# Kernel tuning notes

Measured on AMD Instinct MI355X. Metric: run time of the kernel, lower is better.

The kernel has to match this reference:

```python
import jax, jax.numpy as jnp
import numpy as np

N_ITEMS = 50000
N_USERS = 20000
N_NODES = N_ITEMS + N_USERS
D = 128
N_REL = 3
NNZ = 800000
K_LAYERS = 2
B, S, L = 256, 4, 50


def setup_inputs() -> dict:
    key = jax.random.key(0)
    ks = iter(jax.random.split(key, 40))
    stdv = float(1.0 / np.sqrt(D))

    def uni(shape):
        return jax.random.uniform(next(ks), shape, jnp.float32, -stdv, stdv)

    id_emb = (jax.random.normal(next(ks), (N_ITEMS, D), jnp.float32) * 0.1).at[0].set(0.0)  # padding_idx=0
    user_emb = jax.random.normal(next(ks), (N_USERS, D), jnp.float32) * 0.1
    inp = dict(
        id_emb=id_emb, user_emb=user_emb,
        lin_r_w=uni((K_LAYERS, N_REL, D, D)),
        upi_w=uni((K_LAYERS, D, D)), upi_b=uni((K_LAYERS, D)),
        upu_w=uni((K_LAYERS, D, D)), upu_b=uni((K_LAYERS, D)),
        w_ih=uni((3 * D, 2 * D)), w_hh=uni((3 * D, D)),
        b_ih=uni((3 * D,)), b_hh=uni((3 * D,)),
        b_iah=uni((D,)), b_oah=uni((D,)),
        ei_w=uni((D, D)), ei_b=uni((D,)),
        eo_w=uni((D, D)), eo_b=uni((D,)),
        q1_w=uni((D, D)), q2_w=uni((D, D)), att_w=uni((D,)),
        fuse_w=uni((D, 2 * D)), fuse_b=uni((D,)),
    )
    # global heterogeneous graph: COO per relation over item+user nodes
    inp['rel_rows'] = jax.random.randint(next(ks), (N_REL, NNZ), 0, N_NODES, dtype=jnp.int32)
    inp['rel_cols'] = jax.random.randint(next(ks), (N_REL, NNZ), 0, N_NODES, dtype=jnp.int32)
    inp['rel_vals'] = jax.random.uniform(next(ks), (N_REL, NNZ), jnp.float32) * 0.1
    # session batch: every session has length in [2, L]
    lens = jax.random.randint(next(ks), (B, S), 2, L + 1)
    raw = jax.random.randint(next(ks), (B, S, L), 1, N_ITEMS)
    inp['ids'] = (raw * (jnp.arange(L)[None, None, :] < lens[:, :, None])).astype(jnp.int32)
    inp['uid'] = jax.random.randint(next(ks), (B,), 0, N_USERS, dtype=jnp.int32)
    inp['u_type'] = jax.random.randint(next(ks), (B,), 0, 3).astype(jnp.float32)
    return inp


def _hgnn(h_item, h_user, rel_rows, rel_cols, rel_vals, lin_r_w, upi_w, upi_b, upu_w, upu_b):
    Ni = h_item.shape[0]
    N = Ni + h_user.shape[0]
    for k in range(lin_r_w.shape[0]):
        h_all = jnp.concatenate([h_item, h_user], 0)
        msg = jnp.zeros_like(h_all)
        for r in range(rel_rows.shape[0]):
            Wh = h_all @ lin_r_w[k, r].T  # per-relation linear
            msg = msg + jax.ops.segment_sum(Wh[rel_cols[r]] * rel_vals[r][:, None],
                                            rel_rows[r], num_segments=N)  # sparse.mm
        h_item = jax.nn.relu((msg[:Ni] + h_item) @ upi_w[k].T + upi_b[k])
        h_user = jax.nn.relu((msg[Ni:] + h_user) @ upu_w[k].T + upu_b[k])
    return h_item, h_user


def reference(id_emb, user_emb, lin_r_w, upi_w, upi_b, upu_w, upu_b,
              w_ih, w_hh, b_ih, b_hh, b_iah, b_oah,
              ei_w, ei_b, eo_w, eo_b, q1_w, q2_w, att_w, fuse_w, fuse_b,
              rel_rows, rel_cols, rel_vals, ids, uid, u_type):
    Bb, Ss, Ll = ids.shape
    N = Ss * Bb
    ids_sb = jnp.transpose(ids, (1, 0, 2)).reshape(N, Ll)  # session-major, matches torch concat order
    lens = (ids_sb != 0).sum(-1)  # >= 2 by construction -> all sessions valid
    rows = jnp.arange(N)
    target = ids_sb[rows, lens - 1]
    Lp = Ll - 1
    m_in = jnp.arange(Lp)[None, :] < (lens - 1)[:, None]
    seq_in = ids_sb[:, :Lp] * m_in
    # session graph: consecutive-item edges; in-half sub-diagonal, out-half super-diagonal
    valid = (m_in[:, 1:] & m_in[:, :-1]).astype(jnp.float32)  # [N, Lp-1]
    i1 = jnp.arange(1, Lp)
    i0 = jnp.arange(Lp - 1)
    a_in = jnp.zeros((N, Lp, Lp), jnp.float32).at[:, i1, i0].set(valid)
    a_out = jnp.zeros((N, Lp, Lp), jnp.float32).at[:, i0, i1].set(valid)
    deg = jnp.clip(a_in.sum(-1), 1.0, None)[..., None]
    a_in = a_in / deg
    a_out = a_out / deg
    h = id_emb[seq_in]  # [N, Lp, D]
    # SessionGNN GRU-style cell (step=1)
    m_i = jnp.matmul(a_in, h @ ei_w.T + ei_b) + b_iah
    m_o = jnp.matmul(a_out, h @ eo_w.T + eo_b) + b_oah
    gi = jnp.concatenate([m_i, m_o], -1) @ w_ih.T + b_ih
    gh = h @ w_hh.T + b_hh
    i_r, i_i, i_n = jnp.split(gi, 3, -1)
    h_r, h_i, h_n = jnp.split(gh, 3, -1)
    rg = jax.nn.sigmoid(i_r + h_r)
    zg = jax.nn.sigmoid(i_i + h_i)
    ng = jnp.tanh(i_n + rg * h_n)
    h = ng + zg * (h - ng)
    # attention readout
    ht = h[rows, jnp.clip(lens - 2, 0, None)]
    alpha = jax.nn.sigmoid((ht @ q1_w.T)[:, None, :] + h @ q2_w.T) @ att_w  # [N, Lp]
    alpha = alpha * m_in.astype(jnp.float32)
    alpha = alpha / (alpha.sum(1, keepdims=True) + 1e-8)
    c_cur = jnp.einsum('nl,nld->nd', alpha, h)
    # global HGNN user context
    g_item, g_user = _hgnn(id_emb[:N_ITEMS], user_emb[:N_USERS], rel_rows, rel_cols,
                           rel_vals, lin_r_w, upi_w, upi_b, upu_w, upu_b)
    c_hist = g_user[jnp.tile(uid, Ss)]
    reps = jnp.concatenate([c_cur, c_hist], -1) @ fuse_w.T + fuse_b
    return reps, target, jnp.tile(u_type, Ss)
```

## Files before the change

### kernel.cpp

```cpp
#include <hip/hip_runtime.h>
#include <hip/hip_bf16.h>

typedef __hip_bfloat16 bf16;
typedef unsigned int uint32;
typedef __attribute__((ext_vector_type(8))) short short8;
typedef __attribute__((ext_vector_type(4))) float f32x4;
typedef __attribute__((ext_vector_type(2))) float f32x2;
typedef __attribute__((ext_vector_type(4))) uint32 u32x4;

#define N_ITEMS_C 50000
#define N_USERS_C 20000
#define N_NODES_C 70000
#define NNZ_C 800000
#define NSESS 1024
#define LP 49
#define NTOK (NSESS * LP)
#define NBK 137

__device__ __forceinline__ float bflo(uint32 u) { return __uint_as_float(u << 16); }
__device__ __forceinline__ float bfhi(uint32 u) { return __uint_as_float(u & 0xffff0000u); }
__device__ __forceinline__ float bfhi_fast(uint32 u) { return __uint_as_float(u); }
__device__ __forceinline__ uint32 packbf(float a, float b) {
    return (uint32)__bfloat16_as_ushort(__float2bfloat16(a)) |
           ((uint32)__bfloat16_as_ushort(__float2bfloat16(b)) << 16);
}

__global__ void init_hab_kernel(const float4* __restrict__ idp, const float4* __restrict__ usp,
                                uint32* __restrict__ hab) {
    int i = blockIdx.x * 256 + threadIdx.x;
    float4 w = (i < 1600000) ? idp[i] : usp[i - 1600000];
    uint2 o = make_uint2(packbf(w.x, w.y), packbf(w.z, w.w));
    *(uint2*)&hab[(size_t)i * 2] = o;
}

__global__ __launch_bounds__(256) void bucket_hist_kernel(
    const int* __restrict__ rel_rows, int* __restrict__ bhist)
{
    __shared__ int hist[NBK];
    const int r = blockIdx.y, tid = threadIdx.x;
    if (tid < NBK) hist[tid] = 0;
    __syncthreads();
    const int* rr = rel_rows + (size_t)r * NNZ_C;
#pragma unroll
    for (int i = 0; i < 16; ++i) {
        int e = blockIdx.x * 4096 + i * 256 + tid;
        if (e < NNZ_C) atomicAdd(&hist[rr[e] >> 9], 1);
    }
    __syncthreads();
    if (tid < NBK && hist[tid]) atomicAdd(&bhist[r * NBK + tid], hist[tid]);
}

__global__ __launch_bounds__(256) void bucket_scan_kernel(
    const int* __restrict__ bhist, int* __restrict__ bbase)
{
    __shared__ int s[256];
    const int tid = threadIdx.x;
    for (int r = 0; r < 3; ++r) {
        s[tid] = (tid < NBK) ? bhist[r * NBK + tid] : 0;
        __syncthreads();
        for (int d = 1; d < 256; d <<= 1) {
            int t = (tid >= d) ? s[tid - d] : 0;
            __syncthreads();
            s[tid] += t;
            __syncthreads();
        }
        if (tid < NBK) bbase[r * (NBK + 1) + tid + 1] = s[tid];
        if (tid == 0) bbase[r * (NBK + 1)] = 0;
        __syncthreads();
    }
}

__global__ __launch_bounds__(256) void bucket_scatter_kernel(
    const int* __restrict__ rel_rows, const int* __restrict__ rel_cols,
    const float* __restrict__ rel_vals, const int* __restrict__ bbase,
    int* __restrict__ cursor, int2* __restrict__ tmp)
{
    __shared__ int hist[NBK], gbase[NBK], cur2[NBK];
    const int r = blockIdx.y, tid = threadIdx.x;
    if (tid < NBK) { hist[tid] = 0; cur2[tid] = 0; }
    __syncthreads();
    const int* rr = rel_rows + (size_t)r * NNZ_C;
    const int* rc = rel_cols + (size_t)r * NNZ_C;
    const float* rv = rel_vals + (size_t)r * NNZ_C;
    int rows[16];
#pragma unroll
    for (int i = 0; i < 16; ++i) {
        int e = blockIdx.x * 4096 + i * 256 + tid;
        rows[i] = (e < NNZ_C) ? rr[e] : -1;
        if (rows[i] >= 0) atomicAdd(&hist[rows[i] >> 9], 1);
    }
    __syncthreads();
    if (tid < NBK)
        gbase[tid] = bbase[r * (NBK + 1) + tid] +
                     (hist[tid] ? atomicAdd(&cursor[r * NBK + tid], hist[tid]) : 0);
    __syncthreads();
    int2* tp = tmp + (size_t)r * NNZ_C;
#pragma unroll
    for (int i = 0; i < 16; ++i) {
        int e = blockIdx.x * 4096 + i * 256 + tid;
        if (rows[i] >= 0) {
            int bk = rows[i] >> 9;
            int rank = atomicAdd(&cur2[bk], 1);
            uint32 fb = __float_as_uint(rv[e]);
            uint32 pk = (uint32)rc[e] | (((fb >> 16) & 0x7FFFu) << 17);
            tp[gbase[bk] + rank] = make_int2((int)pk, rows[i]);
        }
    }
}

__global__ __launch_bounds__(256) void bucket_refine_kernel(
    const int2* __restrict__ tmp, const int* __restrict__ bbase,
    int* __restrict__ offs, uint32* __restrict__ edges)
{
    __shared__ int cnt[512], offsL[512], cur[512];
    __shared__ uint32 outb[6656];
    const int b = blockIdx.x, r = blockIdx.y, tid = threadIdx.x;
    const int lane = tid & 63, wid = tid >> 6;
    const int row0 = b << 9;
    const int e0 = bbase[r * (NBK + 1) + b];
    const int e1 = bbase[r * (NBK + 1) + b + 1];
    cnt[tid] = 0; cnt[256 + tid] = 0; cur[tid] = 0; cur[256 + tid] = 0;
    __syncthreads();
    const int2* tp = tmp + (size_t)r * NNZ_C;
    for (int e = e0 + tid; e < e1; e += 256)
        atomicAdd(&cnt[tp[e].y - row0], 1);
    __syncthreads();
    if (wid == 0) {
        int carry = 0;
        for (int c = 0; c < 8; ++c) {
            int x = cnt[c * 64 + lane];
            int inc = x;
#pragma unroll
            for (int d = 1; d < 64; d <<= 1) {
                int y = __shfl_up(inc, d, 64);
                if (lane >= d) inc += y;
            }
            offsL[c * 64 + lane] = inc - x + carry;
            carry += __shfl(inc, 63, 64);
        }
    }
    __syncthreads();
    for (int i = tid; i < 512; i += 256) {
        int row = row0 + i;
        if (row < 70001) offs[(size_t)r * 70001 + row] = e0 + offsL[i];
    }
    for (int e = e0 + tid; e < e1; e += 256) {
        int2 E = tp[e];
        int lr_ = E.y - row0;
        int slot = offsL[lr_] + atomicAdd(&cur[lr_], 1);
        if (slot < 6656) outb[slot] = (uint32)E.x;
    }
    __syncthreads();
    uint32* eo = edges + (size_t)r * NNZ_C + e0;
    for (int i = tid; i < e1 - e0; i += 256) eo[i] = outb[i];
}

__global__ __launch_bounds__(256) void gather_kernel(
    const uint32* __restrict__ hab, const uint32* __restrict__ edges,
    const int* __restrict__ offs, uint32* __restrict__ T)
{
    const int row = blockIdx.x * 4 + (threadIdx.x >> 6);
    const int lane = threadIdx.x & 63;
    const int grp = lane >> 4;
    const int ql  = lane & 15;
    const char* __restrict__ habB = (const char*)hab + ql * 16;
    f32x2 acc[3][4];
#pragma unroll
    for (int r = 0; r < 3; ++r)
#pragma unroll
        for (int j = 0; j < 4; ++j) acc[r][j] = (f32x2){0.f, 0.f};
#pragma unroll
    for (int r = 0; r < 3; ++r) {
        const uint32* __restrict__ ed = edges + (size_t)r * NNZ_C;
        const int* __restrict__ of = offs + (size_t)r * 70001;
        const int e0 = of[row], e1 = of[row + 1];
        if (e0 >= e1) continue;
        const uint32 span = (uint32)(e1 - e0);
        const int s0 = e0 & ~3;
        for (int eb = s0; eb < e1; eb += 16) {
            const int base = eb + grp * 4;
            uint4 E4 = *(const uint4*)&ed[base];
            uint32 Ej0 = ((uint32)(base + 0 - e0) < span) ? E4.x : 0u;
            uint32 Ej1 = ((uint32)(base + 1 - e0) < span) ? E4.y : 0u;
            uint32 Ej2 = ((uint32)(base + 2 - e0) < span) ? E4.z : 0u;
            uint32 Ej3 = ((uint32)(base + 3 - e0) < span) ? E4.w : 0u;
            uint4 u0 = *(const uint4*)(habB + ((Ej0 & 0x1FFFFu) << 8));
            uint4 u1 = *(const uint4*)(habB + ((Ej1 & 0x1FFFFu) << 8));
            uint4 u2 = *(const uint4*)(habB + ((Ej2 & 0x1FFFFu) << 8));
            uint4 u3 = *(const uint4*)(habB + ((Ej3 & 0x1FFFFu) << 8));
            float v0 = __uint_as_float((Ej0 >> 1) & 0x7FFF0000u);
            float v1 = __uint_as_float((Ej1 >> 1) & 0x7FFF0000u);
            float v2 = __uint_as_float((Ej2 >> 1) & 0x7FFF0000u);
            float v3 = __uint_as_float((Ej3 >> 1) & 0x7FFF0000u);
            f32x2 vv;
            vv = (f32x2){v0, v0};
            acc[r][0] += vv * (f32x2){bflo(u0.x), bfhi_fast(u0.x)};
            acc[r][1] += vv * (f32x2){bflo(u0.y), bfhi_fast(u0.y)};
            acc[r][2] += vv * (f32x2){bflo(u0.z), bfhi_fast(u0.z)};
            acc[r][3] += vv * (f32x2){bflo(u0.w), bfhi_fast(u0.w)};
            vv = (f32x2){v1, v1};
            acc[r][0] += vv * (f32x2){bflo(u1.x), bfhi_fast(u1.x)};
            acc[r][1] += vv * (f32x2){bflo(u1.y), bfhi_fast(u1.y)};
            acc[r][2] += vv * (f32x2){bflo(u1.z), bfhi_fast(u1.z)};
            acc[r][3] += vv * (f32x2){bflo(u1.w), bfhi_fast(u1.w)};
            vv = (f32x2){v2, v2};
            acc[r][0] += vv * (f32x2){bflo(u2.x), bfhi_fast(u2.x)};
            acc[r][1] += vv * (f32x2){bflo(u2.y), bfhi_fast(u2.y)};
            acc[r][2] += vv * (f32x2){bflo(u2.z), bfhi_fast(u2.z)};
            acc[r][3] += vv * (f32x2){bflo(u2.w), bfhi_fast(u2.w)};
            vv = (f32x2){v3, v3};
            acc[r][0] += vv * (f32x2){bflo(u3.x), bfhi_fast(u3.x)};
            acc[r][1] += vv * (f32x2){bflo(u3.y), bfhi_fast(u3.y)};
            acc[r][2] += vv * (f32x2){bflo(u3.z), bfhi_fast(u3.z)};
            acc[r][3] += vv * (f32x2){bflo(u3.w), bfhi_fast(u3.w)};
        }
    }
    float* af = (float*)acc;
#pragma unroll
    for (int off = 16; off < 64; off <<= 1)
#pragma unroll
        for (int j = 0; j < 24; ++j) af[j] += __shfl_xor(af[j], off, 64);
    if (grp == 0) {
#pragma unroll
        for (int r = 0; r < 3; ++r) {
            u32x4 o;
            o.x = packbf(acc[r][0].x, acc[r][0].y);
            o.y = packbf(acc[r][1].x, acc[r][1].y);
            o.z = packbf(acc[r][2].x, acc[r][2].y);
            o.w = packbf(acc[r][3].x, acc[r][3].y);
            __builtin_nontemporal_store(o, (u32x4*)&T[(size_t)row * 192 + r * 64 + ql * 4]);
        }
    }
}

__global__ __launch_bounds__(256, 3) void wprep_kernel(
    const float* __restrict__ upi_w, const float* __restrict__ upu_w,
    const float* __restrict__ lin_r_w, int k, uint32* __restrict__ Wcat)
{
    __shared__ float As[128][65];
    __shared__ __align__(8) bf16 Ws[128][66];
    const int which = blockIdx.y, seg = which / 3, r = which % 3;
    const float* U  = (seg == 0 ? upi_w : upu_w) + (size_t)k * 16384;
    const float* Wr = lin_r_w + (size_t)(k * 3 + r) * 16384;
    uint32* out = Wcat + (size_t)seg * 32768;
    const int tid = threadIdx.x;
    const int row0 = blockIdx.x * 64;
#pragma unroll
    for (int i = 0; i < 8; ++i) {
        int id = i * 256 + tid;
        int rr = id >> 5, c4 = (id & 31) << 2;
        float4 v = *(const float4*)&U[(size_t)(row0 + rr) * 128 + c4];
        As[c4][rr] = v.x; As[c4+1][rr] = v.y; As[c4+2][rr] = v.z; As[c4+3][rr] = v.w;
    }
    const int m0 = (tid & 15) * 4;
    const int n0 = (tid >> 4) * 8;
    float acc[4][8];
#pragma unroll
    for (int i = 0; i < 4; ++i)
#pragma unroll
        for (int j = 0; j < 8; ++j) acc[i][j] = 0.f;
    for (int p = 0; p < 2; ++p) {
        if (p) __syncthreads();
        for (int i = 0; i < 32; ++i) {
            int id = i * 256 + tid;
            int c = id >> 6, kf = id & 63;
            Ws[c][kf] = __float2bfloat16(Wr[(size_t)(p * 64 + kf) * 128 + c]);
        }
        __syncthreads();
        for (int k2 = 0; k2 < 32; ++k2) {
            int kk = p * 64 + 2 * k2;
            float av0[4], av1[4];
#pragma unroll
            for (int i = 0; i < 4; ++i) { av0[i] = As[kk][m0 + i]; av1[i] = As[kk + 1][m0 + i]; }
#pragma unroll
            for (int j = 0; j < 8; ++j) {
                uint32 wp = *(const uint32*)&Ws[n0 + j][2 * k2];
                float w0 = bflo(wp), w1 = bfhi(wp);
#pragma unroll
                for (int i = 0; i < 4; ++i)
                    acc[i][j] = fmaf(av1[i], w1, fmaf(av0[i], w0, acc[i][j]));
            }
        }
    }
#pragma unroll
    for (int i = 0; i < 4; ++i) {
        int n = row0 + m0 + i;
#pragma unroll
        for (int j = 0; j < 8; j += 2)
            out[(size_t)n * 256 + (r * 128 + n0 + j) / 2] = packbf(acc[i][j], acc[i][j + 1]);
    }
}

__global__ __launch_bounds__(256) void upack_kernel(
    const float* __restrict__ upi_w, const float* __restrict__ upu_w,
    int k, uint32* __restrict__ Wcat)
{
    int id = blockIdx.x * 256 + threadIdx.x;
    int seg = id >> 13, p = id & 8191;
    int n = p >> 6, j2 = (p & 63);
    const float* U = (seg ? upu_w : upi_w) + (size_t)k * 16384;
    float2 w = *(const float2*)&U[(size_t)n * 128 + j2 * 2];
    Wcat[(size_t)seg * 32768 + (size_t)n * 256 + 192 + j2] = packbf(w.x, w.y);
}

#define HGNN_ITEM_BLOCKS 391
__global__ __launch_bounds__(256) void hgnn_update_mfma_kernel(
    const bf16* __restrict__ T, uint32* __restrict__ hab,
    const bf16* __restrict__ Wcat, const float* __restrict__ upi_b,
    const float* __restrict__ upu_b, int k)
{
    const int tid = threadIdx.x;
    const int wv = tid >> 6, lane = tid & 63, quad = lane >> 4, lr = lane & 15;
    const int bid = blockIdx.x;
    const int seg = (bid >= HGNN_ITEM_BLOCKS) ? 1 : 0;
    const int row0 = seg ? N_ITEMS_C : 0;
    const int M = seg ? N_USERS_C : N_ITEMS_C;
    const int rbase = (seg ? bid - HGNN_ITEM_BLOCKS : bid) * 128;
    const bf16* __restrict__ Wc = Wcat + (size_t)seg * 65536;
    const float* __restrict__ bias = (seg ? upu_b : upi_b) + k * 128;
    const bf16* hb = (const bf16*)hab;
    f32x4 acc[8][2];
#pragma unroll
    for (int mt = 0; mt < 8; ++mt) { acc[mt][0] = (f32x4){0,0,0,0}; acc[mt][1] = (f32x4){0,0,0,0}; }
    int arow[8];
#pragma unroll
    for (int mt = 0; mt < 8; ++mt) {
        int rr = rbase + mt * 16 + lr;
        arow[mt] = row0 + (rr < M ? rr : M - 1);
    }
#pragma unroll
    for (int ks = 0; ks < 16; ++ks) {
        short8 b0 = *(const short8*)&Wc[(size_t)(wv * 32 + lr) * 512 + ks * 32 + quad * 8];
        short8 b1 = *(const short8*)&Wc[(size_t)(wv * 32 + 16 + lr) * 512 + ks * 32 + quad * 8];
#pragma unroll
        for (int mt = 0; mt < 8; ++mt) {
            short8 a;
            if (ks < 12) a = *(const short8*)&T[(size_t)arow[mt] * 384 + ks * 32 + quad * 8];
            else         a = *(const short8*)&hb[(size_t)arow[mt] * 128 + (ks - 12) * 32 + quad * 8];
            acc[mt][0] = __builtin_amdgcn_mfma_f32_16x16x32_bf16(a, b0, acc[mt][0], 0, 0, 0);
            acc[mt][1] = __builtin_amdgcn_mfma_f32_16x16x32_bf16(a, b1, acc[mt][1], 0, 0, 0);
        }
    }
    __syncthreads();
    unsigned short* hw = (unsigned short*)hab;
#pragma unroll
    for (int s = 0; s < 2; ++s) {
        int col = wv * 32 + s * 16 + lr;
        float bv = bias[col];
#pragma unroll
        for (int mt = 0; mt < 8; ++mt)
#pragma unroll
            for (int reg = 0; reg < 4; ++reg) {
                int rr = rbase + mt * 16 + quad * 4 + reg;
                if (rr < M) {
                    float v = fmaxf(acc[mt][s][reg] + bv, 0.f);
                    hw[(size_t)(row0 + rr) * 128 + col] = __bfloat16_as_ushort(__float2bfloat16(v));
                }
            }
    }
}

__global__ __launch_bounds__(256) void mfma_nt_kernel(
    const bf16* __restrict__ A, const int* __restrict__ rowmap,
    const bf16* __restrict__ W0, const float* __restrict__ b0,
    float* __restrict__ O0, int M)
{
    const int tid = threadIdx.x;
    const int wv = tid >> 6, lane = tid & 63, quad = lane >> 4, lr = lane & 15;
    const int rbase = blockIdx.x * 128;
    int arow[8];
#pragma unroll
    for (int mt = 0; mt < 8; ++mt) {
        int rr = rbase + mt * 16 + lr;
        rr = rr < M ? rr : M - 1;
        arow[mt] = rowmap ? rowmap[rr] : rr;
    }
    f32x4 acc0[8][2];
#pragma unroll
    for (int mt = 0; mt < 8; ++mt) { acc0[mt][0] = (f32x4){0,0,0,0}; acc0[mt][1] = (f32x4){0,0,0,0}; }
#pragma unroll
    for (int ks = 0; ks < 4; ++ks) {
        short8 b00 = *(const short8*)&W0[(size_t)(wv * 32 + lr) * 128 + ks * 32 + quad * 8];
        short8 b01 = *(const short8*)&W0[(size_t)(wv * 32 + 16 + lr) * 128 + ks * 32 + quad * 8];
#pragma unroll
        for (int mt = 0; mt < 8; ++mt) {
            short8 a = *(const short8*)&A[(size_t)arow[mt] * 128 + ks * 32 + quad * 8];
            acc0[mt][0] = __builtin_amdgcn_mfma_f32_16x16x32_bf16(a, b00, acc0[mt][0], 0, 0, 0);
            acc0[mt][1] = __builtin_amdgcn_mfma_f32_16x16x32_bf16(a, b01, acc0[mt][1], 0, 0, 0);
        }
    }
#pragma unroll
    for (int s = 0; s < 2; ++s) {
        int col = wv * 32 + s * 16 + lr;
        float bv0 = b0 ? b0[col] : 0.f;
#pragma unroll
        for (int mt = 0; mt < 8; ++mt)
#pragma unroll
            for (int reg = 0; reg < 4; ++reg) {
                int rr = rbase + mt * 16 + quad * 4 + reg;
                if (rr < M) O0[(size_t)rr * 128 + col] = acc0[mt][s][reg] + bv0;
            }
    }
}

__global__ void session_prep_kernel(const int* __restrict__ ids, const int* __restrict__ uid,
                                    const float* __restrict__ u_type,
                                    int* __restrict__ lens, int* __restrict__ rowmap,
                                    float* __restrict__ out_target, float* __restrict__ out_utype)
{
    int n = blockIdx.x * 256 + threadIdx.x;
    if (n >= NSESS) return;
    int b = n & 255, s = n >> 8;
    const int* row = ids + (size_t)(b * 4 + s) * 50;
    int len = 0;
#pragma unroll
    for (int l = 0; l < 50; ++l) len += (row[l] != 0) ? 1 : 0;
    lens[n] = len;
    rowmap[n] = n * LP + (len - 2);
    out_target[n] = (float)row[len - 1];
    out_utype[n] = u_type[b];
}

__global__ void chist_kernel(const uint32* __restrict__ hab, const int* __restrict__ uid,
                             float* __restrict__ chist) {
    int n = blockIdx.x, d = threadIdx.x;
    uint32 u = hab[(size_t)(N_ITEMS_C + uid[n & 255]) * 64 + (d >> 1)];
    chist[(size_t)n * 128 + d] = (d & 1) ? bfhi(u) : bflo(u);
}

__global__ __launch_bounds__(256) void h0_gather_kernel(
    const float* __restrict__ id_emb, const int* __restrict__ ids,
    const int* __restrict__ lens, uint32* __restrict__ hb) {
    int g = blockIdx.x * 4 + (threadIdx.x >> 6);
    int d = threadIdx.x & 63;
    int n = g / LP;
    int tt = g - n * LP;
    int len = lens[n];
    int b = n & 255, s = n >> 8;
    int id = (tt < len - 1) ? ids[(size_t)(b * 4 + s) * 50 + tt] : 0;
    float2 e = *(const float2*)&id_emb[(size_t)id * 128 + d * 2];
    hb[(size_t)g * 64 + d] = packbf(e.x, e.y);
}

__global__ __launch_bounds__(256) void epack_kernel(
    const float* __restrict__ w_ih, const float* __restrict__ w_hh,
    const float* __restrict__ ei_w, const float* __restrict__ eo_w,
    const float* __restrict__ q2_w, const float* __restrict__ q1_w,
    const float* __restrict__ fuse_w, uint32* __restrict__ dst)
{
    int id = blockIdx.x * 256 + threadIdx.x;
    if (id >= 106496) {
        if (id >= 139264) return;
        int f = id - 106496;
        int kk = f >> 7, n = f & 127;
        ((float*)dst)[id] = fuse_w[(size_t)n * 256 + kk];
        return;
    }
    const float* src; int off;
    if      (id <  49152) { src = w_ih; off = id; }
    else if (id <  73728) { src = w_hh; off = id - 49152; }
    else if (id <  81920) { src = ei_w; off = id - 73728; }
    else if (id <  90112) { src = eo_w; off = id - 81920; }
    else if (id <  98304) { src = q2_w; off = id - 90112; }
    else                  { src = q1_w; off = id - 98304; }
    float2 w = *(const float2*)&src[(size_t)off * 2];
    dst[id] = packbf(w.x, w.y);
}

__global__ __launch_bounds__(256) void gru_fused_kernel(
    const uint32* __restrict__ hb,
    unsigned short* __restrict__ hb2,
    const bf16* __restrict__ Wi, const bf16* __restrict__ Wo,
    const bf16* __restrict__ wihb,
    const bf16* __restrict__ whhb,
    const float* __restrict__ ei_b, const float* __restrict__ eo_b,
    const float* __restrict__ b_iah, const float* __restrict__ b_oah,
    const float* __restrict__ b_ih, const float* __restrict__ b_hh,
    const int* __restrict__ lens)
{
    __shared__ __align__(16) bf16 Agi[32][264];
    const int tid = threadIdx.x;
    const int wv = tid >> 6;
    const int lane = tid & 63;
    const int quad = lane >> 4;
    const int lr = lane & 15;
    const int c0 = wv * 32;
    const int g0 = blockIdx.x * 32;
    const bf16* hbb = (const bf16*)hb;

    int arows[4];
#pragma unroll
    for (int t = 0; t < 4; ++t) {
        int r = g0 + (t - 1) * 16 + lr;
        arows[t] = (r < 0) ? r + NTOK : (r >= NTOK ? r - NTOK : r);
    }
    f32x4 aEi[3][2], aEo[3][2];
#pragma unroll
    for (int t = 0; t < 3; ++t) {
        aEi[t][0] = (f32x4){0,0,0,0}; aEi[t][1] = (f32x4){0,0,0,0};
        aEo[t][0] = (f32x4){0,0,0,0}; aEo[t][1] = (f32x4){0,0,0,0};
    }
#pragma unroll
    for (int ks = 0; ks < 4; ++ks) {
        short8 bi0 = *(const short8*)&Wi[(size_t)(wv * 32 + lr) * 128 + ks * 32 + quad * 8];
        short8 bi1 = *(const short8*)&Wi[(size_t)(wv * 32 + 16 + lr) * 128 + ks * 32 + quad * 8];
        short8 bo0 = *(const short8*)&Wo[(size_t)(wv * 32 + lr) * 128 + ks * 32 + quad * 8];
        short8 bo1 = *(const short8*)&Wo[(size_t)(wv * 32 + 16 + lr) * 128 + ks * 32 + quad * 8];
        short8 a[4];
#pragma unroll
        for (int t = 0; t < 4; ++t)
            a[t] = *(const short8*)&hbb[(size_t)arows[t] * 128 + ks * 32 + quad * 8];
#pragma unroll
        for (int t = 0; t < 3; ++t) {
            aEi[t][0] = __builtin_amdgcn_mfma_f32_16x16x32_bf16(a[t], bi0, aEi[t][0], 0, 0, 0);
            aEi[t][1] = __builtin_amdgcn_mfma_f32_16x16x32_bf16(a[t], bi1, aEi[t][1], 0, 0, 0);
            aEo[t][0] = __builtin_amdgcn_mfma_f32_16x16x32_bf16(a[t + 1], bo0, aEo[t][0], 0, 0, 0);
            aEo[t][1] = __builtin_amdgcn_mfma_f32_16x16x32_bf16(a[t + 1], bo1, aEo[t][1], 0, 0, 0);
        }
    }
#pragma unroll
    for (int s = 0; s < 2; ++s) {
        int col = c0 + s * 16 + lr;
        float bei = ei_b[col], beo = eo_b[col];
        float bia = b_iah[col], boa = b_oah[col];
#pragma unroll
        for (int t = 0; t < 3; ++t)
#pragma unroll
            for (int reg = 0; reg < 4; ++reg) {
                int src = g0 + (t - 1) * 16 + quad * 4 + reg;
                int ssrc = (src < 0) ? src + NTOK : (src >= NTOK ? src - NTOK : src);
                int d1 = ssrc + 1; if (d1 == NTOK) d1 = 0;
                int ld = d1 - g0;
                if ((unsigned)ld < 32u) {
                    int n1 = d1 / LP, t1 = d1 - n1 * LP, l1 = lens[n1];
                    float v = bia + ((t1 >= 1 && t1 < l1 - 1) ? aEi[t][s][reg] + bei : 0.f);
                    Agi[ld][col] = __float2bfloat16(v);
                }
                int src2 = g0 + t * 16 + quad * 4 + reg;
                int ssrc2 = (src2 >= NTOK) ? src2 - NTOK : src2;
                int d2 = (ssrc2 == 0) ? NTOK - 1 : ssrc2 - 1;
                int ld2 = d2 - g0;
                if ((unsigned)ld2 < 32u) {
                    int n2 = d2 / LP, t2 = d2 - n2 * LP, l2 = lens[n2];
                    float v = boa + ((t2 < l2 - 2) ? aEo[t][s][reg] + beo : 0.f);
                    Agi[ld2][128 + col] = __float2bfloat16(v);
                }
            }
    }
    __syncthreads();

    int arow[2];
#pragma unroll
    for (int mt = 0; mt < 2; ++mt) arow[mt] = g0 + mt * 16 + lr;
    f32x4 acc[2][2][4];
#pragma unroll
    for (int mt = 0; mt < 2; ++mt)
#pragma unroll
        for (int s = 0; s < 2; ++s)
#pragma unroll
            for (int j = 0; j < 4; ++j) acc[mt][s][j] = (f32x4){0.f, 0.f, 0.f, 0.f};

#pragma unroll 2
    for (int ks = 0; ks < 8; ++ks) {
        short8 bfr[2][3];
#pragma unroll
        for (int s = 0; s < 2; ++s)
#pragma unroll
            for (int gte = 0; gte < 3; ++gte) {
                int n0 = gte * 128 + c0 + s * 16 + lr;
                bfr[s][gte] = *(const short8*)&wihb[(size_t)n0 * 256 + ks * 32 + quad * 8];
            }
#pragma unroll
        for (int mt = 0; mt < 2; ++mt) {
            short8 a = *(const short8*)&Agi[mt * 16 + lr][ks * 32 + quad * 8];
#pragma unroll
            for (int s = 0; s < 2; ++s) {
                acc[mt][s][0] = __builtin_amdgcn_mfma_f32_16x16x32_bf16(a, bfr[s][0], acc[mt][s][0], 0, 0, 0);
                acc[mt][s][1] = __builtin_amdgcn_mfma_f32_16x16x32_bf16(a, bfr[s][1], acc[mt][s][1], 0, 0, 0);
                acc[mt][s][2] = __builtin_amdgcn_mfma_f32_16x16x32_bf16(a, bfr[s][2], acc[mt][s][2], 0, 0, 0);
            }
        }
    }
#pragma unroll 2
    for (int ks = 0; ks < 4; ++ks) {
        short8 bfr[2][3];
#pragma unroll
        for (int s = 0; s < 2; ++s)
#pragma unroll
            for (int gte = 0; gte < 3; ++gte) {
                int n0 = gte * 128 + c0 + s * 16 + lr;
                bfr[s][gte] = *(const short8*)&whhb[(size_t)n0 * 128 + ks * 32 + quad * 8];
            }
#pragma unroll
        for (int mt = 0; mt < 2; ++mt) {
            short8 a = *(const short8*)&hbb[(size_t)arow[mt] * 128 + ks * 32 + quad * 8];
#pragma unroll
            for (int s = 0; s < 2; ++s) {
                acc[mt][s][0] = __builtin_amdgcn_mfma_f32_16x16x32_bf16(a, bfr[s][0], acc[mt][s][0], 0, 0, 0);
                acc[mt][s][1] = __builtin_amdgcn_mfma_f32_16x16x32_bf16(a, bfr[s][1], acc[mt][s][1], 0, 0, 0);
                acc[mt][s][3] = __builtin_amdgcn_mfma_f32_16x16x32_bf16(a, bfr[s][2], acc[mt][s][3], 0, 0, 0);
            }
        }
    }

    const unsigned short* hold = (const unsigned short*)hb;
#pragma unroll
    for (int s = 0; s < 2; ++s) {
        int col = c0 + s * 16 + lr;
        float brz = b_ih[col] + b_hh[col];
        float bzz = b_ih[col + 128] + b_hh[col + 128];
        float bin = b_ih[col + 256];
        float bhn = b_hh[col + 256];
#pragma unroll
        for (int mt = 0; mt < 2; ++mt)
#pragma unroll
            for (int reg = 0; reg < 4; ++reg) {
                int row = g0 + mt * 16 + quad * 4 + reg;
                float rg = 1.f / (1.f + expf(-(acc[mt][s][0][reg] + brz)));
                float zg = 1.f / (1.f + expf(-(acc[mt][s][1][reg] + bzz)));
                float ng = tanhf(acc[mt][s][2][reg] + bin + rg * (acc[mt][s][3][reg] + bhn));
                size_t idx = (size_t)row * 128 + col;
                float ho = __uint_as_float((uint32)hold[idx] << 16);
                hb2[idx] = __bfloat16_as_ushort(__float2bfloat16(ng + zg * (ho - ng)));
            }
    }
}

__global__ __launch_bounds__(256) void alpha_kernel(
    const float* __restrict__ q1h, const float* __restrict__ q2h,
    const float* __restrict__ att_w, const int* __restrict__ lens,
    float* __restrict__ al)
{
    int tok = blockIdx.x * 4 + (threadIdx.x >> 6);
    int lane = threadIdx.x & 63;
    int n = tok / LP, t = tok - n * LP;
    int len = lens[n];
    float2 q2 = *(const float2*)&q2h[(size_t)tok * 128 + lane * 2];
    float2 q1 = *(const float2*)&q1h[(size_t)n * 128 + lane * 2];
    float2 aw = *(const float2*)&att_w[lane * 2];
    float s = aw.x / (1.f + expf(-(q1.x + q2.x))) + aw.y / (1.f + expf(-(q1.y + q2.y)));
#pragma unroll
    for (int off = 1; off < 64; off <<= 1) s += __shfl_xor(s, off, 64);
    if (lane == 0) al[tok] = (t < len - 1) ? s : 0.f;
}

__global__ __launch_bounds__(128) void attn_fuse_kernel(
    const float* __restrict__ alG, const unsigned short* __restrict__ hu,
    const float* __restrict__ chist, const int* __restrict__ lens,
    const float* __restrict__ ftwf, const float* __restrict__ fuse_b,
    float* __restrict__ out)
{
    __shared__ float al[64], cv[256];
    const int n = blockIdx.x, tid = threadIdx.x;
    if (tid < 64) al[tid] = (tid < LP) ? alG[(size_t)n * LP + tid] : 0.f;
    __syncthreads();
    const int len = lens[n];
    float ssum = 0.f;
    for (int t = 0; t < len - 1; ++t) ssum += al[t];
    float inv = 1.f / (ssum + 1e-8f);
    float c = 0.f;
    for (int t = 0; t < len - 1; ++t) {
        float hv = __uint_as_float((uint32)hu[(size_t)(n * LP + t) * 128 + tid] << 16);
        c += al[t] * inv * hv;
    }
    cv[tid] = c;
    cv[128 + tid] = chist[(size_t)n * 128 + tid];
    __syncthreads();
    float s = fuse_b[tid];
    for (int kk = 0; kk < 256; ++kk)
        s += cv[kk] * ftwf[(size_t)kk * 128 + tid];
    out[(size_t)n * 128 + tid] = s;
}

extern "C" void kernel_launch(void* const* d_in, const int* in_sizes, int n_in,
                              void* d_out, int out_size, void* d_ws, size_t ws_size,
                              hipStream_t stream)
{
    const float* id_emb   = (const float*)d_in[0];
    const float* user_emb = (const float*)d_in[1];
    const float* lin_r_w  = (const float*)d_in[2];
    const float* upi_w    = (const float*)d_in[3];
    const float* upi_b    = (const float*)d_in[4];
    const float* upu_w    = (const float*)d_in[5];
    const float* upu_b    = (const float*)d_in[6];
    const float* w_ih     = (const float*)d_in[7];
    const float* w_hh     = (const float*)d_in[8];
    const float* b_ih     = (const float*)d_in[9];
    const float* b_hh     = (const float*)d_in[10];
    const float* b_iah    = (const float*)d_in[11];
    const float* b_oah    = (const float*)d_in[12];
    const float* ei_w     = (const float*)d_in[13];
    const float* ei_b     = (const float*)d_in[14];
    const float* eo_w     = (const float*)d_in[15];
    const float* eo_b     = (const float*)d_in[16];
    const float* q1_w     = (const float*)d_in[17];
    const float* q2_w     = (const float*)d_in[18];
    const float* att_w    = (const float*)d_in[19];
    const float* fuse_w   = (const float*)d_in[20];
    const float* fuse_b   = (const float*)d_in[21];
    const int*  rel_rows  = (const int*)d_in[22];
    const int*  rel_cols  = (const int*)d_in[23];
    const float* rel_vals = (const float*)d_in[24];
    const int*  ids       = (const int*)d_in[25];
    const int*  uid       = (const int*)d_in[26];
    const float* u_type   = (const float*)d_in[27];
    float* out = (float*)d_out;

    uint32* W32    = (uint32*)d_ws;
    uint32* hab    = W32;
    uint32* T      = W32 + 4480000;
    uint32* edges  = W32 + 17920000;
    int2*   tmp    = (int2*)(W32 + 20320000);
    int*    offs   = (int*)(W32 + 25120000);
    int*    bhist  = (int*)(W32 + 25330004);
    int*    cursor = (int*)(W32 + 25330415);
    int*    bbase  = (int*)(W32 + 25330826);
    uint32* Wcat   = W32 + 25331240;
    float*  q1h    = (float*)(W32 + 25396776);
    float*  chist  = (float*)(W32 + 25527848);
    int*    lens   = (int*)(W32 + 25658920);
    int*    rowmap = (int*)(W32 + 25659944);
    float*  alG    = (float*)(W32 + 25660968);
    uint32* sess_hb = W32;
    float* q2h      = (float*)(W32 + 4480000);
    unsigned short* hb2 = (unsigned short*)(W32 + 10902528);
    uint32* wpk     = W32 + 17920000;
    uint32* wihb = wpk;
    uint32* whhb = wpk + 49152;
    uint32* eiwb = wpk + 73728;
    uint32* eowb = wpk + 81920;
    uint32* q2wb = wpk + 90112;
    uint32* q1wb = wpk + 98304;
    float*  ftwf = (float*)(wpk + 106496);
    if (ws_size < (size_t)27144192 * 4 + 4096) return;

    init_hab_kernel<<<8750, 256, 0, stream>>>((const float4*)id_emb, (const float4*)user_emb, hab);
    hipMemsetAsync(bhist, 0, (size_t)822 * 4, stream);
    bucket_hist_kernel<<<dim3(196, 3), 256, 0, stream>>>(rel_rows, bhist);
    bucket_scan_kernel<<<1, 256, 0, stream>>>(bhist, bbase);
    bucket_scatter_kernel<<<dim3(196, 3), 256, 0, stream>>>(rel_rows, rel_cols, rel_vals,
                                                            bbase, cursor, tmp);
    bucket_refine_kernel<<<dim3(NBK, 3), 256, 0, stream>>>(tmp, bbase, offs, edges);

    for (int k = 0; k < 2; ++k) {
        wprep_kernel<<<dim3(2, 6), 256, 0, stream>>>(upi_w, upu_w, lin_r_w, k, Wcat);
        upack_kernel<<<64, 256, 0, stream>>>(upi_w, upu_w, k, Wcat);
        gather_kernel<<<17500, 256, 0, stream>>>(hab, edges, offs, T);
        hgnn_update_mfma_kernel<<<548, 256, 0, stream>>>((const bf16*)T, hab,
            (const bf16*)Wcat, upi_b, upu_b, k);
    }

    session_prep_kernel<<<4, 256, 0, stream>>>(ids, uid, u_type, lens, rowmap,
        out + 131072, out + 132096);
    chist_kernel<<<NSESS, 128, 0, stream>>>(hab, uid, chist);
    epack_kernel<<<544, 256, 0, stream>>>(w_ih, w_hh, ei_w, eo_w, q2_w, q1_w, fuse_w, wpk);
    h0_gather_kernel<<<NTOK / 4, 256, 0, stream>>>(id_emb, ids, lens, sess_hb);
    gru_fused_kernel<<<1568, 256, 0, stream>>>(sess_hb, hb2,
        (const bf16*)eiwb, (const bf16*)eowb,
        (const bf16*)wihb, (const bf16*)whhb,
        ei_b, eo_b, b_iah, b_oah, b_ih, b_hh, lens);
    mfma_nt_kernel<<<392, 256, 0, stream>>>((const bf16*)hb2, nullptr,
        (const bf16*)q2wb, nullptr, q2h, NTOK);
    mfma_nt_kernel<<<8, 256, 0, stream>>>((const bf16*)hb2, rowmap,
        (const bf16*)q1wb, nullptr, q1h, NSESS);
    alpha_kernel<<<NTOK / 4, 256, 0, stream>>>(q1h, q2h, att_w, lens, alG);
    attn_fuse_kernel<<<NSESS, 128, 0, stream>>>(alG, (const unsigned short*)hb2,
        chist, lens, ftwf, fuse_b, out);
}
```

Baseline: 748.2 us.

## Fuse q2 projection with alpha scoring and merge small prep kernels

Fuses the q2 GEMM with the sigmoid/attention-weight reduction so the NTOK×128 fp32 q2h intermediate is never written or read back. Merges init_hab with bucket histogram, and session prep, chist, weight packing and h0 gather into single launches. Weight prep for both HGNN layers is hoisted out of the loop into one launch each, and h0 gather computes length with a ballot. The aim is fewer launches and less memory traffic, at the cost of buffer relocation in the workspace and more divergent monolithic kernels.

```diff
diff --git a/kernel.cpp b/kernel.cpp
--- a/kernel.cpp
+++ b/kernel.cpp
@@ -25,25 +25,27 @@
            ((uint32)__bfloat16_as_ushort(__float2bfloat16(b)) << 16);
 }
 
-__global__ void init_hab_kernel(const float4* __restrict__ idp, const float4* __restrict__ usp,
-                                uint32* __restrict__ hab) {
-    int i = blockIdx.x * 256 + threadIdx.x;
-    float4 w = (i < 1600000) ? idp[i] : usp[i - 1600000];
-    uint2 o = make_uint2(packbf(w.x, w.y), packbf(w.z, w.w));
-    *(uint2*)&hab[(size_t)i * 2] = o;
-}
-
-__global__ __launch_bounds__(256) void bucket_hist_kernel(
-    const int* __restrict__ rel_rows, int* __restrict__ bhist)
+__global__ __launch_bounds__(256) void init_hist_kernel(
+    const float4* __restrict__ idp, const float4* __restrict__ usp,
+    uint32* __restrict__ hab, const int* __restrict__ rel_rows, int* __restrict__ bhist)
 {
     __shared__ int hist[NBK];
-    const int r = blockIdx.y, tid = threadIdx.x;
+    const int tid = threadIdx.x;
+    if (blockIdx.x < 8750) {
+        int i = blockIdx.x * 256 + tid;
+        float4 w = (i < 1600000) ? idp[i] : usp[i - 1600000];
+        uint2 o = make_uint2(packbf(w.x, w.y), packbf(w.z, w.w));
+        *(uint2*)&hab[(size_t)i * 2] = o;
+        return;
+    }
+    const int hb = blockIdx.x - 8750;
+    const int r = hb / 196, xb = hb - r * 196;
     if (tid < NBK) hist[tid] = 0;
     __syncthreads();
     const int* rr = rel_rows + (size_t)r * NNZ_C;
 #pragma unroll
     for (int i = 0; i < 16; ++i) {
-        int e = blockIdx.x * 4096 + i * 256 + tid;
+        int e = xb * 4096 + i * 256 + tid;
         if (e < NNZ_C) atomicAdd(&hist[rr[e] >> 9], 1);
     }
     __syncthreads();
@@ -235,14 +237,15 @@
 
 __global__ __launch_bounds__(256, 3) void wprep_kernel(
     const float* __restrict__ upi_w, const float* __restrict__ upu_w,
-    const float* __restrict__ lin_r_w, int k, uint32* __restrict__ Wcat)
+    const float* __restrict__ lin_r_w, uint32* __restrict__ Wcat)
 {
     __shared__ float As[128][65];
     __shared__ __align__(8) bf16 Ws[128][66];
     const int which = blockIdx.y, seg = which / 3, r = which % 3;
+    const int k = blockIdx.z;
     const float* U  = (seg == 0 ? upi_w : upu_w) + (size_t)k * 16384;
     const float* Wr = lin_r_w + (size_t)(k * 3 + r) * 16384;
-    uint32* out = Wcat + (size_t)seg * 32768;
+    uint32* out = Wcat + (size_t)(k * 2 + seg) * 32768;
     const int tid = threadIdx.x;
     const int row0 = blockIdx.x * 64;
 #pragma unroll
@@ -293,14 +296,15 @@
 
 __global__ __launch_bounds__(256) void upack_kernel(
     const float* __restrict__ upi_w, const float* __restrict__ upu_w,
-    int k, uint32* __restrict__ Wcat)
+    uint32* __restrict__ Wcat)
 {
     int id = blockIdx.x * 256 + threadIdx.x;
-    int seg = id >> 13, p = id & 8191;
+    int k = id >> 14, rest = id & 16383;
+    int seg = rest >> 13, p = rest & 8191;
     int n = p >> 6, j2 = (p & 63);
     const float* U = (seg ? upu_w : upi_w) + (size_t)k * 16384;
     float2 w = *(const float2*)&U[(size_t)n * 128 + j2 * 2];
-    Wcat[(size_t)seg * 32768 + (size_t)n * 256 + 192 + j2] = packbf(w.x, w.y);
+    Wcat[(size_t)(k * 2 + seg) * 32768 + (size_t)n * 256 + 192 + j2] = packbf(w.x, w.y);
 }
 
 #define HGNN_ITEM_BLOCKS 391
@@ -316,7 +320,7 @@
     const int row0 = seg ? N_ITEMS_C : 0;
     const int M = seg ? N_USERS_C : N_ITEMS_C;
     const int rbase = (seg ? bid - HGNN_ITEM_BLOCKS : bid) * 128;
-    const bf16* __restrict__ Wc = Wcat + (size_t)seg * 65536;
+    const bf16* __restrict__ Wc = Wcat + (size_t)(k * 2 + seg) * 65536;
     const float* __restrict__ bias = (seg ? upu_b : upi_b) + k * 128;
     const bf16* hb = (const bf16*)hab;
     f32x4 acc[8][2];
@@ -403,68 +407,73 @@
     }
 }
 
-__global__ void session_prep_kernel(const int* __restrict__ ids, const int* __restrict__ uid,
-                                    const float* __restrict__ u_type,
-                                    int* __restrict__ lens, int* __restrict__ rowmap,
-                                    float* __restrict__ out_target, float* __restrict__ out_utype)
-{
-    int n = blockIdx.x * 256 + threadIdx.x;
-    if (n >= NSESS) return;
-    int b = n & 255, s = n >> 8;
-    const int* row = ids + (size_t)(b * 4 + s) * 50;
-    int len = 0;
-#pragma unroll
-    for (int l = 0; l < 50; ++l) len += (row[l] != 0) ? 1 : 0;
-    lens[n] = len;
-    rowmap[n] = n * LP + (len - 2);
-    out_target[n] = (float)row[len - 1];
-    out_utype[n] = u_type[b];
-}
-
-__global__ void chist_kernel(const uint32* __restrict__ hab, const int* __restrict__ uid,
-                             float* __restrict__ chist) {
-    int n = blockIdx.x, d = threadIdx.x;
-    uint32 u = hab[(size_t)(N_ITEMS_C + uid[n & 255]) * 64 + (d >> 1)];
-    chist[(size_t)n * 128 + d] = (d & 1) ? bfhi(u) : bflo(u);
-}
-
-__global__ __launch_bounds__(256) void h0_gather_kernel(
-    const float* __restrict__ id_emb, const int* __restrict__ ids,
-    const int* __restrict__ lens, uint32* __restrict__ hb) {
-    int g = blockIdx.x * 4 + (threadIdx.x >> 6);
-    int d = threadIdx.x & 63;
-    int n = g / LP;
-    int tt = g - n * LP;
-    int len = lens[n];
-    int b = n & 255, s = n >> 8;
-    int id = (tt < len - 1) ? ids[(size_t)(b * 4 + s) * 50 + tt] : 0;
-    float2 e = *(const float2*)&id_emb[(size_t)id * 128 + d * 2];
-    hb[(size_t)g * 64 + d] = packbf(e.x, e.y);
-}
-
-__global__ __launch_bounds__(256) void epack_kernel(
+__global__ __launch_bounds__(256) void misc_prep_kernel(
+    const int* __restrict__ ids, const int* __restrict__ uid,
+    const float* __restrict__ u_type, const float* __restrict__ id_emb,
+    const uint32* __restrict__ hab,
     const float* __restrict__ w_ih, const float* __restrict__ w_hh,
     const float* __restrict__ ei_w, const float* __restrict__ eo_w,
     const float* __restrict__ q2_w, const float* __restrict__ q1_w,
-    const float* __restrict__ fuse_w, uint32* __restrict__ dst)
-{
-    int id = blockIdx.x * 256 + threadIdx.x;
-    if (id >= 106496) {
-        if (id >= 139264) return;
-        int f = id - 106496;
-        int kk = f >> 7, n = f & 127;
-        ((float*)dst)[id] = fuse_w[(size_t)n * 256 + kk];
+    const float* __restrict__ fuse_w,
+    int* __restrict__ lens, int* __restrict__ rowmap,
+    float* __restrict__ out_target, float* __restrict__ out_utype,
+    float* __restrict__ chist, uint32* __restrict__ wdst,
+    uint32* __restrict__ hb)
+{
+    const int bid = blockIdx.x, tid = threadIdx.x;
+    if (bid < 4) {
+        int n = bid * 256 + tid;
+        if (n >= NSESS) return;
+        int b = n & 255, s = n >> 8;
+        const int* row = ids + (size_t)(b * 4 + s) * 50;
+        int len = 0;
+#pragma unroll
+        for (int l = 0; l < 50; ++l) len += (row[l] != 0) ? 1 : 0;
+        lens[n] = len;
+        rowmap[n] = n * LP + (len - 2);
+        out_target[n] = (float)row[len - 1];
+        out_utype[n] = u_type[b];
         return;
     }
-    const float* src; int off;
-    if      (id <  49152) { src = w_ih; off = id; }
-    else if (id <  73728) { src = w_hh; off = id - 49152; }
-    else if (id <  81920) { src = ei_w; off = id - 73728; }
-    else if (id <  90112) { src = eo_w; off = id - 81920; }
-    else if (id <  98304) { src = q2_w; off = id - 90112; }
-    else                  { src = q1_w; off = id - 98304; }
-    float2 w = *(const float2*)&src[(size_t)off * 2];
-    dst[id] = packbf(w.x, w.y);
+    if (bid < 516) {
+        int n = (bid - 4) * 2 + (tid >> 7);
+        int d = tid & 127;
+        uint32 u = hab[(size_t)(N_ITEMS_C + uid[n & 255]) * 64 + (d >> 1)];
+        chist[(size_t)n * 128 + d] = (d & 1) ? bfhi(u) : bflo(u);
+        return;
+    }
+    if (bid < 1060) {
+        int id = (bid - 516) * 256 + tid;
+        if (id >= 106496) {
+            if (id >= 139264) return;
+            int f = id - 106496;
+            int kk = f >> 7, n = f & 127;
+            ((float*)wdst)[id] = fuse_w[(size_t)n * 256 + kk];
+            return;
+        }
+        const float* src; int off;
+        if      (id <  49152) { src = w_ih; off = id; }
+        else if (id <  73728) { src = w_hh; off = id - 49152; }
+        else if (id <  81920) { src = ei_w; off = id - 73728; }
+        else if (id <  90112) { src = eo_w; off = id - 81920; }
+        else if (id <  98304) { src = q2_w; off = id - 90112; }
+        else                  { src = q1_w; off = id - 98304; }
+        float2 w = *(const float2*)&src[(size_t)off * 2];
+        wdst[id] = packbf(w.x, w.y);
+        return;
+    }
+    int g = (bid - 1060) * 4 + (tid >> 6);
+    int d = tid & 63;
+    int n = g / LP;
+    int tt = g - n * LP;
+    int b = n & 255, s = n >> 8;
+    const int* row = ids + (size_t)(b * 4 + s) * 50;
+    int v = (d < 50) ? row[d] : 0;
+    unsigned long long bal = __ballot(v != 0);
+    int len = __popcll(bal);
+    int id0 = (tt < len - 1) ? row[tt] : 0;
+    float2 e = *(const float2*)&id_emb[(size_t)id0 * 128 + d * 2];
+    hb[(size_t)g * 64 + d] = packbf(e.x, e.y);
 }
 
 __global__ __launch_bounds__(256) void gru_fused_kernel(
@@ -626,22 +635,55 @@
     }
 }
 
-__global__ __launch_bounds__(256) void alpha_kernel(
-    const float* __restrict__ q1h, const float* __restrict__ q2h,
-    const float* __restrict__ att_w, const int* __restrict__ lens,
-    float* __restrict__ al)
-{
-    int tok = blockIdx.x * 4 + (threadIdx.x >> 6);
-    int lane = threadIdx.x & 63;
-    int n = tok / LP, t = tok - n * LP;
-    int len = lens[n];
-    float2 q2 = *(const float2*)&q2h[(size_t)tok * 128 + lane * 2];
-    float2 q1 = *(const float2*)&q1h[(size_t)n * 128 + lane * 2];
-    float2 aw = *(const float2*)&att_w[lane * 2];
-    float s = aw.x / (1.f + expf(-(q1.x + q2.x))) + aw.y / (1.f + expf(-(q1.y + q2.y)));
-#pragma unroll
-    for (int off = 1; off < 64; off <<= 1) s += __shfl_xor(s, off, 64);
-    if (lane == 0) al[tok] = (t < len - 1) ? s : 0.f;
+__global__ __launch_bounds__(256) void q2alpha_kernel(
+    const bf16* __restrict__ A,
+    const bf16* __restrict__ W0,
+    const float* __restrict__ q1h, const float* __restrict__ att_w,
+    const int* __restrict__ lens, float* __restrict__ alG)
+{
+    __shared__ float red[4][128];
+    const int tid = threadIdx.x;
+    const int wv = tid >> 6, lane = tid & 63, quad = lane >> 4, lr = lane & 15;
+    const int rbase = blockIdx.x * 128;
+    f32x4 acc0[8][2];
+#pragma unroll
+    for (int mt = 0; mt < 8; ++mt) { acc0[mt][0] = (f32x4){0,0,0,0}; acc0[mt][1] = (f32x4){0,0,0,0}; }
+#pragma unroll
+    for (int ks = 0; ks < 4; ++ks) {
+        short8 b00 = *(const short8*)&W0[(size_t)(wv * 32 + lr) * 128 + ks * 32 + quad * 8];
+        short8 b01 = *(const short8*)&W0[(size_t)(wv * 32 + 16 + lr) * 128 + ks * 32 + quad * 8];
+#pragma unroll
+        for (int mt = 0; mt < 8; ++mt) {
+            short8 a = *(const short8*)&A[(size_t)(rbase + mt * 16 + lr) * 128 + ks * 32 + quad * 8];
+            acc0[mt][0] = __builtin_amdgcn_mfma_f32_16x16x32_bf16(a, b00, acc0[mt][0], 0, 0, 0);
+            acc0[mt][1] = __builtin_amdgcn_mfma_f32_16x16x32_bf16(a, b01, acc0[mt][1], 0, 0, 0);
+        }
+    }
+    const int colA = wv * 32 + lr, colB = colA + 16;
+    const float awA = att_w[colA], awB = att_w[colB];
+#pragma unroll
+    for (int mt = 0; mt < 8; ++mt)
+#pragma unroll
+        for (int reg = 0; reg < 4; ++reg) {
+            int row = rbase + mt * 16 + quad * 4 + reg;
+            int n = row / LP;
+            float q1A = q1h[(size_t)n * 128 + colA];
+            float q1B = q1h[(size_t)n * 128 + colB];
+            float p = awA / (1.f + expf(-(q1A + acc0[mt][0][reg])))
+                    + awB / (1.f + expf(-(q1B + acc0[mt][1][reg])));
+            p += __shfl_xor(p, 1, 64);
+            p += __shfl_xor(p, 2, 64);
+            p += __shfl_xor(p, 4, 64);
+            p += __shfl_xor(p, 8, 64);
+            if (lr == 0) red[wv][mt * 16 + quad * 4 + reg] = p;
+        }
+    __syncthreads();
+    if (tid < 128) {
+        int row = rbase + tid;
+        int n = row / LP, t = row - n * LP;
+        float s = red[0][tid] + red[1][tid] + red[2][tid] + red[3][tid];
+        alG[row] = (t < lens[n] - 1) ? s : 0.f;
+    }
 }
 
 __global__ __launch_bounds__(128) void attn_fuse_kernel(
@@ -715,14 +757,13 @@
     int*    bhist  = (int*)(W32 + 25330004);
     int*    cursor = (int*)(W32 + 25330415);
     int*    bbase  = (int*)(W32 + 25330826);
-    uint32* Wcat   = W32 + 25331240;
     float*  q1h    = (float*)(W32 + 25396776);
     float*  chist  = (float*)(W32 + 25527848);
     int*    lens   = (int*)(W32 + 25658920);
     int*    rowmap = (int*)(W32 + 25659944);
     float*  alG    = (float*)(W32 + 25660968);
-    uint32* sess_hb = W32;
-    float* q2h      = (float*)(W32 + 4480000);
+    uint32* Wcat   = W32 + 25711144;
+    uint32* sess_hb = W32 + 20320000;
     unsigned short* hb2 = (unsigned short*)(W32 + 10902528);
     uint32* wpk     = W32 + 17920000;
     uint32* wihb = wpk;
@@ -734,36 +775,34 @@
     float*  ftwf = (float*)(wpk + 106496);
     if (ws_size < (size_t)27144192 * 4 + 4096) return;
 
-    init_hab_kernel<<<8750, 256, 0, stream>>>((const float4*)id_emb, (const float4*)user_emb, hab);
     hipMemsetAsync(bhist, 0, (size_t)822 * 4, stream);
-    bucket_hist_kernel<<<dim3(196, 3), 256, 0, stream>>>(rel_rows, bhist);
+    init_hist_kernel<<<9338, 256, 0, stream>>>((const float4*)id_emb, (const float4*)user_emb,
+                                               hab, rel_rows, bhist);
     bucket_scan_kernel<<<1, 256, 0, stream>>>(bhist, bbase);
     bucket_scatter_kernel<<<dim3(196, 3), 256, 0, stream>>>(rel_rows, rel_cols, rel_vals,
                                                             bbase, cursor, tmp);
     bucket_refine_kernel<<<dim3(NBK, 3), 256, 0, stream>>>(tmp, bbase, offs, edges);
 
+    wprep_kernel<<<dim3(2, 6, 2), 256, 0, stream>>>(upi_w, upu_w, lin_r_w, Wcat);
+    upack_kernel<<<128, 256, 0, stream>>>(upi_w, upu_w, Wcat);
+
     for (int k = 0; k < 2; ++k) {
-        wprep_kernel<<<dim3(2, 6), 256, 0, stream>>>(upi_w, upu_w, lin_r_w, k, Wcat);
-        upack_kernel<<<64, 256, 0, stream>>>(upi_w, upu_w, k, Wcat);
         gather_kernel<<<17500, 256, 0, stream>>>(hab, edges, offs, T);
         hgnn_update_mfma_kernel<<<548, 256, 0, stream>>>((const bf16*)T, hab,
             (const bf16*)Wcat, upi_b, upu_b, k);
     }
 
-    session_prep_kernel<<<4, 256, 0, stream>>>(ids, uid, u_type, lens, rowmap,
-        out + 131072, out + 132096);
-    chist_kernel<<<NSESS, 128, 0, stream>>>(hab, uid, chist);
-    epack_kernel<<<544, 256, 0, stream>>>(w_ih, w_hh, ei_w, eo_w, q2_w, q1_w, fuse_w, wpk);
-    h0_gather_kernel<<<NTOK / 4, 256, 0, stream>>>(id_emb, ids, lens, sess_hb);
+    misc_prep_kernel<<<13604, 256, 0, stream>>>(ids, uid, u_type, id_emb, hab,
+        w_ih, w_hh, ei_w, eo_w, q2_w, q1_w, fuse_w,
+        lens, rowmap, out + 131072, out + 132096, chist, wpk, sess_hb);
     gru_fused_kernel<<<1568, 256, 0, stream>>>(sess_hb, hb2,
         (const bf16*)eiwb, (const bf16*)eowb,
         (const bf16*)wihb, (const bf16*)whhb,
         ei_b, eo_b, b_iah, b_oah, b_ih, b_hh, lens);
-    mfma_nt_kernel<<<392, 256, 0, stream>>>((const bf16*)hb2, nullptr,
-        (const bf16*)q2wb, nullptr, q2h, NTOK);
     mfma_nt_kernel<<<8, 256, 0, stream>>>((const bf16*)hb2, rowmap,
         (const bf16*)q1wb, nullptr, q1h, NSESS);
-    alpha_kernel<<<NTOK / 4, 256, 0, stream>>>(q1h, q2h, att_w, lens, alG);
+    q2alpha_kernel<<<392, 256, 0, stream>>>((const bf16*)hb2, (const bf16*)q2wb,
+        q1h, att_w, lens, alG);
     attn_fuse_kernel<<<NSESS, 128, 0, stream>>>(alG, (const unsigned short*)hb2,
         chist, lens, ftwf, fuse_b, out);
 }
```

Measured after the change: 710.1 us. 5.1% less time.
